# Performance work log

Hardware: AMD Instinct MI355X
Metric: run time of the kernel (lower is better)

## Reference

```python
import jax, jax.numpy as jnp
import numpy as np

NUM_USER, NUM_ITEM, NUM_TIME = 200000, 100000, 5000
P, Q, R = 32, 32, 32
N = 131072


def _xavier(key, shape):
    fan_in, fan_out = shape[0], int(np.prod(shape[1:]))
    limit = float(np.sqrt(6.0 / (fan_in + fan_out)))
    return jax.random.uniform(key, shape, dtype=jnp.float32, minval=-limit, maxval=limit)


def setup_inputs() -> dict:
    key = jax.random.key(0)
    k1, k2, k3, k4, k5, k6, k7 = jax.random.split(key, 7)
    return {
        "i_input": jax.random.randint(k1, (N,), 0, NUM_USER),
        "j_input": jax.random.randint(k2, (N,), 0, NUM_ITEM),
        "k_input": jax.random.randint(k3, (N,), 0, NUM_TIME),
        "user_embeddings": _xavier(k4, (NUM_USER, P)),
        "item_embeddings": _xavier(k5, (NUM_ITEM, Q)),
        "time_embeddings": _xavier(k6, (NUM_TIME, R)),
        "core_tensor": _xavier(k7, (P, Q, R)),
    }


def reference(i_input, j_input, k_input, user_embeddings, item_embeddings,
              time_embeddings, core_tensor):
    # Gather per-sample embeddings: [n,p], [n,q], [n,r]
    i_embeds = user_embeddings[i_input]
    j_embeds = item_embeddings[j_input]
    k_embeds = time_embeddings[k_input]
    # Fused Tucker contraction: never materialize the (n,p,q,r) outer product.
    # Mathematically identical to einsum('np,nq,nr,pqr->n', ...).
    t = jnp.einsum('np,pqr->nqr', i_embeds, core_tensor)  # [n,q,r]
    t = jnp.einsum('nqr,nq->nr', t, j_embeds)             # [n,r]
    return jnp.einsum('nr,nr->n', t, k_embeds)            # [n]
```

## Files before the change

kernel.cpp:

```cpp
#include <hip/hip_runtime.h>


#define BIN_CAP 128

__global__ __launch_bounds__(256) void build_H(const float* __restrict__ G,
                                               const float* __restrict__ W,
                                               float* __restrict__ H,
                                               int num_time) {
    const int pq4 = threadIdx.x;
    const int kbase = blockIdx.x * 8;

    float acc[8][4];
#pragma unroll
    for (int kk = 0; kk < 8; ++kk)
#pragma unroll
        for (int i = 0; i < 4; ++i) acc[kk][i] = 0.f;

#pragma unroll
    for (int r4 = 0; r4 < 8; ++r4) {
        float4 g[4];
#pragma unroll
        for (int i = 0; i < 4; ++i)
            g[i] = *(const float4*)(G + (size_t)(pq4 * 4 + i) * 32 + r4 * 4);
#pragma unroll
        for (int kk = 0; kk < 8; ++kk) {
            int k = kbase + kk;
            int kc = (k < num_time) ? k : (num_time - 1);
            float4 w = *(const float4*)(W + (size_t)kc * 32 + r4 * 4);
#pragma unroll
            for (int i = 0; i < 4; ++i)
                acc[kk][i] += g[i].x * w.x + g[i].y * w.y + g[i].z * w.z + g[i].w * w.w;
        }
    }

#pragma unroll
    for (int kk = 0; kk < 8; ++kk) {
        int k = kbase + kk;
        if (k < num_time) {
            float4 o = make_float4(acc[kk][0], acc[kk][1], acc[kk][2], acc[kk][3]);
            *(float4*)(H + (size_t)k * 1024 + pq4 * 4) = o;
        }
    }
}

__global__ __launch_bounds__(256) void scatter_k(const int* __restrict__ K,
                                                 const int* __restrict__ I,
                                                 const int* __restrict__ J,
                                                 int* __restrict__ counts,
                                                 int4* __restrict__ bins,
                                                 int* __restrict__ ovf_cnt,
                                                 int4* __restrict__ ovf,
                                                 int n) {
    for (int idx = blockIdx.x * blockDim.x + threadIdx.x; idx < n;
         idx += gridDim.x * blockDim.x) {
        int k = K[idx];
        int4 rec = make_int4(idx, I[idx], J[idx], k);
        int pos = atomicAdd(&counts[k], 1);
        if (pos < BIN_CAP) {
            bins[(size_t)k * BIN_CAP + pos] = rec;
        } else {
            int o = atomicAdd(ovf_cnt, 1);
            ovf[o] = rec;
        }
    }
}

__global__ __launch_bounds__(256) void tucker_eval_grouped(
        const float* __restrict__ U, const float* __restrict__ V,
        const float* __restrict__ H, const int* __restrict__ counts,
        const int4* __restrict__ bins, float* __restrict__ out,
        int num_time) {
    __shared__ float4 Hs4[4][256];
    const int wave = threadIdx.x >> 6;
    const int lane = threadIdx.x & 63;
    const int k = blockIdx.x * 4 + wave;
    const int qq = lane & 7;
    const int s8 = lane >> 3;

    int m = 0;
    if (k < num_time) {
        const float4* __restrict__ Hrow4 = (const float4*)(H + (size_t)k * 1024);
#pragma unroll
        for (int c = 0; c < 4; ++c)
            Hs4[wave][lane + 64 * c] = Hrow4[lane + 64 * c];
        m = counts[k];
        m = (m < BIN_CAP) ? m : BIN_CAP;
    }
    __syncthreads();
    if (k >= num_time || m == 0) return;

    const int iters = (m + 7) >> 3;
    const float4* __restrict__ Hw = Hs4[wave];

    for (int t = 0; t < iters; ++t) {
        const int s = t * 8 + s8;
        if (s < m) {
            int4 rec = bins[(size_t)k * BIN_CAP + s];
            const float4* __restrict__ Ur = (const float4*)(U + (size_t)rec.y * 32);
            float4 u[8];
#pragma unroll
            for (int p4 = 0; p4 < 8; ++p4) u[p4] = Ur[p4];
            float4 v4 = ((const float4*)(V + (size_t)rec.z * 32))[qq];

            float4 acc = make_float4(0.f, 0.f, 0.f, 0.f);
#pragma unroll
            for (int p4 = 0; p4 < 8; ++p4) {
                float4 h;
                h = Hw[(p4 * 4 + 0) * 8 + qq];
                acc.x += u[p4].x * h.x; acc.y += u[p4].x * h.y;
                acc.z += u[p4].x * h.z; acc.w += u[p4].x * h.w;
                h = Hw[(p4 * 4 + 1) * 8 + qq];
                acc.x += u[p4].y * h.x; acc.y += u[p4].y * h.y;
                acc.z += u[p4].y * h.z; acc.w += u[p4].y * h.w;
                h = Hw[(p4 * 4 + 2) * 8 + qq];
                acc.x += u[p4].z * h.x; acc.y += u[p4].z * h.y;
                acc.z += u[p4].z * h.z; acc.w += u[p4].z * h.w;
                h = Hw[(p4 * 4 + 3) * 8 + qq];
                acc.x += u[p4].w * h.x; acc.y += u[p4].w * h.y;
                acc.z += u[p4].w * h.z; acc.w += u[p4].w * h.w;
            }
            float sd = acc.x * v4.x + acc.y * v4.y + acc.z * v4.z + acc.w * v4.w;
            sd += __shfl_xor(sd, 1, 64);
            sd += __shfl_xor(sd, 2, 64);
            sd += __shfl_xor(sd, 4, 64);
            if (qq == 0) out[rec.x] = sd;
        }
    }
}

__global__ __launch_bounds__(256) void tucker_eval_overflow(
        const float* __restrict__ U, const float* __restrict__ V,
        const float* __restrict__ H, const int* __restrict__ ovf_cnt,
        const int4* __restrict__ ovf, float* __restrict__ out) {
    const int gwave = (int)((blockIdx.x * (unsigned)blockDim.x + threadIdx.x) >> 6);
    const int nwaves = (int)((gridDim.x * (unsigned)blockDim.x) >> 6);
    const int lane = threadIdx.x & 63;
    const int qq = lane & 7;
    const int pg = lane >> 3;
    const int cnt = *ovf_cnt;

    for (int s = gwave; s < cnt; s += nwaves) {
        int4 rec = ovf[s];
        const float4* __restrict__ Hrow = (const float4*)(H + (size_t)rec.w * 1024);
        const float* __restrict__ Ur = U + (size_t)rec.y * 32;

        float4 acc = make_float4(0.f, 0.f, 0.f, 0.f);
#pragma unroll
        for (int it = 0; it < 4; ++it) {
            float4 h = Hrow[lane + it * 64];
            float up = Ur[pg + it * 8];
            acc.x += up * h.x; acc.y += up * h.y;
            acc.z += up * h.z; acc.w += up * h.w;
        }
#pragma unroll
        for (int off = 8; off < 64; off <<= 1) {
            acc.x += __shfl_xor(acc.x, off, 64);
            acc.y += __shfl_xor(acc.y, off, 64);
            acc.z += __shfl_xor(acc.z, off, 64);
            acc.w += __shfl_xor(acc.w, off, 64);
        }
        float4 v4 = ((const float4*)(V + (size_t)rec.z * 32))[qq];
        float sd = acc.x * v4.x + acc.y * v4.y + acc.z * v4.z + acc.w * v4.w;
        sd += __shfl_xor(sd, 1, 64);
        sd += __shfl_xor(sd, 2, 64);
        sd += __shfl_xor(sd, 4, 64);
        if (lane == 0) out[rec.x] = sd;
    }
}

__global__ __launch_bounds__(256) void tucker_eval(const int* __restrict__ I,
                                                   const int* __restrict__ J,
                                                   const int* __restrict__ K,
                                                   const float* __restrict__ U,
                                                   const float* __restrict__ V,
                                                   const float* __restrict__ H,
                                                   float* __restrict__ out,
                                                   int n_samples) {
    const int wave = (int)((blockIdx.x * (unsigned)blockDim.x + threadIdx.x) >> 6);
    const int lane = threadIdx.x & 63;
    if (wave >= n_samples) return;
    const int i = I[wave];
    const int j = J[wave];
    const int k = K[wave];
    const int qq = lane & 7;
    const int pg = lane >> 3;
    const float4* __restrict__ Hrow = (const float4*)(H + (size_t)k * 1024);
    const float* __restrict__ Urow = U + (size_t)i * 32;
    float4 acc = make_float4(0.f, 0.f, 0.f, 0.f);
#pragma unroll
    for (int it = 0; it < 4; ++it) {
        float4 h = Hrow[lane + it * 64];
        float up = Urow[pg + it * 8];
        acc.x += up * h.x; acc.y += up * h.y;
        acc.z += up * h.z; acc.w += up * h.w;
    }
#pragma unroll
    for (int off = 8; off < 64; off <<= 1) {
        acc.x += __shfl_xor(acc.x, off, 64);
        acc.y += __shfl_xor(acc.y, off, 64);
        acc.z += __shfl_xor(acc.z, off, 64);
        acc.w += __shfl_xor(acc.w, off, 64);
    }
    float4 v4 = ((const float4*)(V + (size_t)j * 32))[qq];
    float s = acc.x * v4.x + acc.y * v4.y + acc.z * v4.z + acc.w * v4.w;
    s += __shfl_xor(s, 1, 64);
    s += __shfl_xor(s, 2, 64);
    s += __shfl_xor(s, 4, 64);
    if (lane == 0) out[wave] = s;
}

__global__ __launch_bounds__(256) void tucker_direct(const int* __restrict__ I,
                                                     const int* __restrict__ J,
                                                     const int* __restrict__ K,
                                                     const float* __restrict__ U,
                                                     const float* __restrict__ V,
                                                     const float* __restrict__ W,
                                                     const float* __restrict__ G,
                                                     float* __restrict__ out,
                                                     int n_samples) {
    __shared__ float Gc[4 * 32 * 32];
    const int n = blockIdx.x * blockDim.x + threadIdx.x;
    const bool active = (n < n_samples);
    int i = 0, j = 0, k = 0;
    if (active) { i = I[n]; j = J[n]; k = K[n]; }
    float4 w4[8];
#pragma unroll
    for (int r4 = 0; r4 < 8; ++r4)
        w4[r4] = ((const float4*)(W + (size_t)k * 32))[r4];
    float v[32];
#pragma unroll
    for (int q4 = 0; q4 < 8; ++q4) {
        float4 t = ((const float4*)(V + (size_t)j * 32))[q4];
        v[q4 * 4 + 0] = t.x; v[q4 * 4 + 1] = t.y;
        v[q4 * 4 + 2] = t.z; v[q4 * 4 + 3] = t.w;
    }
    const float* __restrict__ Urow = U + (size_t)i * 32;
    float acc = 0.f;
    for (int c = 0; c < 8; ++c) {
        __syncthreads();
#pragma unroll
        for (int t = 0; t < 4; ++t) {
            int idx = threadIdx.x + t * 256;
            ((float4*)Gc)[idx] = ((const float4*)(G + (size_t)c * 4096))[idx];
        }
        __syncthreads();
        for (int pp = 0; pp < 4; ++pp) {
            float up = Urow[c * 4 + pp];
#pragma unroll
            for (int q = 0; q < 32; ++q) {
                float t0 = 0.f;
#pragma unroll
                for (int r4 = 0; r4 < 8; ++r4) {
                    float4 g = ((const float4*)Gc)[pp * 256 + q * 8 + r4];
                    t0 += g.x * w4[r4].x + g.y * w4[r4].y + g.z * w4[r4].z + g.w * w4[r4].w;
                }
                acc += up * v[q] * t0;
            }
        }
    }
    if (active) out[n] = acc;
}

extern "C" void kernel_launch(void* const* d_in, const int* in_sizes, int n_in,
                              void* d_out, int out_size, void* d_ws, size_t ws_size,
                              hipStream_t stream) {
    const int*   I = (const int*)d_in[0];
    const int*   J = (const int*)d_in[1];
    const int*   K = (const int*)d_in[2];
    const float* U = (const float*)d_in[3];
    const float* V = (const float*)d_in[4];
    const float* W = (const float*)d_in[5];
    const float* G = (const float*)d_in[6];
    float* out = (float*)d_out;

    const int n_samples = in_sizes[0];
    const int num_time = in_sizes[5] / 32;

    const size_t h_bytes = (size_t)num_time * 1024 * sizeof(float);
    const size_t z_bytes = (size_t)(num_time + 1) * sizeof(int);
    const size_t z_pad = (z_bytes + 15) & ~(size_t)15;
    const size_t bins_bytes = (size_t)num_time * BIN_CAP * sizeof(int4);
    const size_t ovf_bytes = (size_t)n_samples * sizeof(int4);
    const size_t need_full = h_bytes + z_pad + bins_bytes + ovf_bytes;

    if (ws_size >= need_full) {
        float* H       = (float*)d_ws;
        int*   counts  = (int*)((char*)d_ws + h_bytes);
        int*   ovf_cnt = counts + num_time;
        int4*  bins    = (int4*)((char*)d_ws + h_bytes + z_pad);
        int4*  ovf     = (int4*)((char*)d_ws + h_bytes + z_pad + bins_bytes);

        hipMemsetAsync(counts, 0, z_bytes, stream);
        scatter_k<<<512, 256, 0, stream>>>(K, I, J, counts, bins, ovf_cnt, ovf,
                                           n_samples);
        build_H<<<(num_time + 7) / 8, 256, 0, stream>>>(G, W, H, num_time);
        tucker_eval_grouped<<<(num_time + 3) / 4, 256, 0, stream>>>(
            U, V, H, counts, bins, out, num_time);
        tucker_eval_overflow<<<64, 256, 0, stream>>>(U, V, H, ovf_cnt, ovf, out);
    } else if (ws_size >= h_bytes) {
        float* H = (float*)d_ws;
        build_H<<<(num_time + 7) / 8, 256, 0, stream>>>(G, W, H, num_time);
        const long long total_threads = (long long)n_samples * 64;
        tucker_eval<<<(int)((total_threads + 255) / 256), 256, 0, stream>>>(
            I, J, K, U, V, H, out, n_samples);
    } else {
        tucker_direct<<<(n_samples + 255) / 256, 256, 0, stream>>>(
            I, J, K, U, V, W, G, out, n_samples);
    }
}
```

Before: 136.6 us.

## Fuse scatter with H build and fold overflow pass into grouped eval

Merges the sample-binning scatter and the per-time H precompute into one launch, using a block-index split so the two independent jobs run concurrently. The overflow evaluation moves into the tail of the grouped eval kernel, dropping a separate launch. The grouped loop is also split into full 8-sample iterations plus one guarded remainder. Together these cut two kernel launches and the serialisation between them. The cost is a heterogeneous kernel whose register use is set by the heavier build path, and the overflow work now runs on every grouped block after its own bins are done.

Measured after the change: 137.1 us, median of 2. Within noise of the previous version (+0.4%).

```diff
diff --git a/kernel.cpp b/kernel.cpp
--- a/kernel.cpp
+++ b/kernel.cpp
@@ -3,64 +3,61 @@
 
 #define BIN_CAP 128
 
-__global__ __launch_bounds__(256) void build_H(const float* __restrict__ G,
-                                               const float* __restrict__ W,
-                                               float* __restrict__ H,
-                                               int num_time) {
-    const int pq4 = threadIdx.x;
-    const int kbase = blockIdx.x * 8;
-
-    float acc[8][4];
-#pragma unroll
-    for (int kk = 0; kk < 8; ++kk)
-#pragma unroll
-        for (int i = 0; i < 4; ++i) acc[kk][i] = 0.f;
-
-#pragma unroll
-    for (int r4 = 0; r4 < 8; ++r4) {
-        float4 g[4];
-#pragma unroll
-        for (int i = 0; i < 4; ++i)
-            g[i] = *(const float4*)(G + (size_t)(pq4 * 4 + i) * 32 + r4 * 4);
+__global__ __launch_bounds__(256) void scatter_build(
+        const int* __restrict__ K, const int* __restrict__ I,
+        const int* __restrict__ J, const float* __restrict__ G,
+        const float* __restrict__ W, int* __restrict__ counts,
+        int4* __restrict__ bins, int* __restrict__ ovf_cnt,
+        int4* __restrict__ ovf, float* __restrict__ H,
+        int n, int num_time, int n_scatter_blocks) {
+    if ((int)blockIdx.x < n_scatter_blocks) {
+        const int idx = blockIdx.x * 256 + threadIdx.x;
+        if (idx < n) {
+            int k = K[idx];
+            int4 rec = make_int4(idx, I[idx], J[idx], k);
+            int pos = atomicAdd(&counts[k], 1);
+            if (pos < BIN_CAP) {
+                bins[(size_t)k * BIN_CAP + pos] = rec;
+            } else {
+                int o = atomicAdd(ovf_cnt, 1);
+                ovf[o] = rec;
+            }
+        }
+    } else {
+        const int pq4 = threadIdx.x;
+        const int kbase = ((int)blockIdx.x - n_scatter_blocks) * 8;
+
+        float acc[8][4];
+#pragma unroll
+        for (int kk = 0; kk < 8; ++kk)
+#pragma unroll
+            for (int i = 0; i < 4; ++i) acc[kk][i] = 0.f;
+
+#pragma unroll
+        for (int r4 = 0; r4 < 8; ++r4) {
+            float4 g[4];
+#pragma unroll
+            for (int i = 0; i < 4; ++i)
+                g[i] = *(const float4*)(G + (size_t)(pq4 * 4 + i) * 32 + r4 * 4);
+#pragma unroll
+            for (int kk = 0; kk < 8; ++kk) {
+                int k = kbase + kk;
+                int kc = (k < num_time) ? k : (num_time - 1);
+                float4 w = *(const float4*)(W + (size_t)kc * 32 + r4 * 4);
+#pragma unroll
+                for (int i = 0; i < 4; ++i)
+                    acc[kk][i] += g[i].x * w.x + g[i].y * w.y +
+                                  g[i].z * w.z + g[i].w * w.w;
+            }
+        }
+
 #pragma unroll
         for (int kk = 0; kk < 8; ++kk) {
             int k = kbase + kk;
-            int kc = (k < num_time) ? k : (num_time - 1);
-            float4 w = *(const float4*)(W + (size_t)kc * 32 + r4 * 4);
-#pragma unroll
-            for (int i = 0; i < 4; ++i)
-                acc[kk][i] += g[i].x * w.x + g[i].y * w.y + g[i].z * w.z + g[i].w * w.w;
-        }
-    }
-
-#pragma unroll
-    for (int kk = 0; kk < 8; ++kk) {
-        int k = kbase + kk;
-        if (k < num_time) {
-            float4 o = make_float4(acc[kk][0], acc[kk][1], acc[kk][2], acc[kk][3]);
-            *(float4*)(H + (size_t)k * 1024 + pq4 * 4) = o;
-        }
-    }
-}
-
-__global__ __launch_bounds__(256) void scatter_k(const int* __restrict__ K,
-                                                 const int* __restrict__ I,
-                                                 const int* __restrict__ J,
-                                                 int* __restrict__ counts,
-                                                 int4* __restrict__ bins,
-                                                 int* __restrict__ ovf_cnt,
-                                                 int4* __restrict__ ovf,
-                                                 int n) {
-    for (int idx = blockIdx.x * blockDim.x + threadIdx.x; idx < n;
-         idx += gridDim.x * blockDim.x) {
-        int k = K[idx];
-        int4 rec = make_int4(idx, I[idx], J[idx], k);
-        int pos = atomicAdd(&counts[k], 1);
-        if (pos < BIN_CAP) {
-            bins[(size_t)k * BIN_CAP + pos] = rec;
-        } else {
-            int o = atomicAdd(ovf_cnt, 1);
-            ovf[o] = rec;
+            if (k < num_time) {
+                float4 o = make_float4(acc[kk][0], acc[kk][1], acc[kk][2], acc[kk][3]);
+                *(float4*)(H + (size_t)k * 1024 + pq4 * 4) = o;
+            }
         }
     }
 }
@@ -68,7 +65,8 @@
 __global__ __launch_bounds__(256) void tucker_eval_grouped(
         const float* __restrict__ U, const float* __restrict__ V,
         const float* __restrict__ H, const int* __restrict__ counts,
-        const int4* __restrict__ bins, float* __restrict__ out,
+        const int4* __restrict__ bins, const int* __restrict__ ovf_cnt,
+        const int4* __restrict__ ovf, float* __restrict__ out,
         int num_time) {
     __shared__ float4 Hs4[4][256];
     const int wave = threadIdx.x >> 6;
@@ -87,15 +85,15 @@
         m = (m < BIN_CAP) ? m : BIN_CAP;
     }
     __syncthreads();
-    if (k >= num_time || m == 0) return;
-
-    const int iters = (m + 7) >> 3;
-    const float4* __restrict__ Hw = Hs4[wave];
-
-    for (int t = 0; t < iters; ++t) {
-        const int s = t * 8 + s8;
-        if (s < m) {
-            int4 rec = bins[(size_t)k * BIN_CAP + s];
+
+    if (k < num_time && m > 0) {
+        const float4* __restrict__ Hw = Hs4[wave];
+        const int4* __restrict__ binsk = bins + (size_t)k * BIN_CAP;
+        const int full = m >> 3;
+
+        for (int t = 0; t < full; ++t) {
+            const int s = t * 8 + s8;
+            int4 rec = binsk[s];
             const float4* __restrict__ Ur = (const float4*)(U + (size_t)rec.y * 32);
             float4 u[8];
 #pragma unroll
@@ -125,46 +123,110 @@
             sd += __shfl_xor(sd, 4, 64);
             if (qq == 0) out[rec.x] = sd;
         }
-    }
-}
-
-__global__ __launch_bounds__(256) void tucker_eval_overflow(
-        const float* __restrict__ U, const float* __restrict__ V,
-        const float* __restrict__ H, const int* __restrict__ ovf_cnt,
-        const int4* __restrict__ ovf, float* __restrict__ out) {
-    const int gwave = (int)((blockIdx.x * (unsigned)blockDim.x + threadIdx.x) >> 6);
-    const int nwaves = (int)((gridDim.x * (unsigned)blockDim.x) >> 6);
-    const int lane = threadIdx.x & 63;
-    const int qq = lane & 7;
-    const int pg = lane >> 3;
+
+        const int s = full * 8 + s8;
+        if (s < m) {
+            int4 rec = binsk[s];
+            const float4* __restrict__ Ur = (const float4*)(U + (size_t)rec.y * 32);
+            float4 u[8];
+#pragma unroll
+            for (int p4 = 0; p4 < 8; ++p4) u[p4] = Ur[p4];
+            float4 v4 = ((const float4*)(V + (size_t)rec.z * 32))[qq];
+
+            float4 acc = make_float4(0.f, 0.f, 0.f, 0.f);
+#pragma unroll
+            for (int p4 = 0; p4 < 8; ++p4) {
+                float4 h;
+                h = Hw[(p4 * 4 + 0) * 8 + qq];
+                acc.x += u[p4].x * h.x; acc.y += u[p4].x * h.y;
+                acc.z += u[p4].x * h.z; acc.w += u[p4].x * h.w;
+                h = Hw[(p4 * 4 + 1) * 8 + qq];
+                acc.x += u[p4].y * h.x; acc.y += u[p4].y * h.y;
+                acc.z += u[p4].y * h.z; acc.w += u[p4].y * h.w;
+                h = Hw[(p4 * 4 + 2) * 8 + qq];
+                acc.x += u[p4].z * h.x; acc.y += u[p4].z * h.y;
+                acc.z += u[p4].z * h.z; acc.w += u[p4].z * h.w;
+                h = Hw[(p4 * 4 + 3) * 8 + qq];
+                acc.x += u[p4].w * h.x; acc.y += u[p4].w * h.y;
+                acc.z += u[p4].w * h.z; acc.w += u[p4].w * h.w;
+            }
+            float sd = acc.x * v4.x + acc.y * v4.y + acc.z * v4.z + acc.w * v4.w;
+            sd += __shfl_xor(sd, 1, 64);
+            sd += __shfl_xor(sd, 2, 64);
+            sd += __shfl_xor(sd, 4, 64);
+            if (qq == 0) out[rec.x] = sd;
+        }
+    }
+
     const int cnt = *ovf_cnt;
-
-    for (int s = gwave; s < cnt; s += nwaves) {
-        int4 rec = ovf[s];
-        const float4* __restrict__ Hrow = (const float4*)(H + (size_t)rec.w * 1024);
-        const float* __restrict__ Ur = U + (size_t)rec.y * 32;
-
-        float4 acc = make_float4(0.f, 0.f, 0.f, 0.f);
-#pragma unroll
-        for (int it = 0; it < 4; ++it) {
-            float4 h = Hrow[lane + it * 64];
-            float up = Ur[pg + it * 8];
-            acc.x += up * h.x; acc.y += up * h.y;
-            acc.z += up * h.z; acc.w += up * h.w;
-        }
-#pragma unroll
-        for (int off = 8; off < 64; off <<= 1) {
-            acc.x += __shfl_xor(acc.x, off, 64);
-            acc.y += __shfl_xor(acc.y, off, 64);
-            acc.z += __shfl_xor(acc.z, off, 64);
-            acc.w += __shfl_xor(acc.w, off, 64);
-        }
-        float4 v4 = ((const float4*)(V + (size_t)rec.z * 32))[qq];
-        float sd = acc.x * v4.x + acc.y * v4.y + acc.z * v4.z + acc.w * v4.w;
-        sd += __shfl_xor(sd, 1, 64);
-        sd += __shfl_xor(sd, 2, 64);
-        sd += __shfl_xor(sd, 4, 64);
-        if (lane == 0) out[rec.x] = sd;
+    if (cnt > 0) {
+        const int pg = lane >> 3;
+        const int gwave = blockIdx.x * 4 + wave;
+        const int nwaves = gridDim.x * 4;
+        for (int s = gwave; s < cnt; s += nwaves) {
+            int4 rec = ovf[s];
+            const float4* __restrict__ Hrow = (const float4*)(H + (size_t)rec.w * 1024);
+            const float* __restrict__ Ur = U + (size_t)rec.y * 32;
+
+            float4 acc = make_float4(0.f, 0.f, 0.f, 0.f);
+#pragma unroll
+            for (int it = 0; it < 4; ++it) {
+                float4 h = Hrow[lane + it * 64];
+                float up = Ur[pg + it * 8];
+                acc.x += up * h.x; acc.y += up * h.y;
+                acc.z += up * h.z; acc.w += up * h.w;
+            }
+#pragma unroll
+            for (int off = 8; off < 64; off <<= 1) {
+                acc.x += __shfl_xor(acc.x, off, 64);
+                acc.y += __shfl_xor(acc.y, off, 64);
+                acc.z += __shfl_xor(acc.z, off, 64);
+                acc.w += __shfl_xor(acc.w, off, 64);
+            }
+            float4 v4 = ((const float4*)(V + (size_t)rec.z * 32))[qq];
+            float sd = acc.x * v4.x + acc.y * v4.y + acc.z * v4.z + acc.w * v4.w;
+            sd += __shfl_xor(sd, 1, 64);
+            sd += __shfl_xor(sd, 2, 64);
+            sd += __shfl_xor(sd, 4, 64);
+            if (lane == 0) out[rec.x] = sd;
+        }
+    }
+}
+
+__global__ __launch_bounds__(256) void build_H(const float* __restrict__ G,
+                                               const float* __restrict__ W,
+                                               float* __restrict__ H,
+                                               int num_time) {
+    const int pq4 = threadIdx.x;
+    const int kbase = blockIdx.x * 8;
+    float acc[8][4];
+#pragma unroll
+    for (int kk = 0; kk < 8; ++kk)
+#pragma unroll
+        for (int i = 0; i < 4; ++i) acc[kk][i] = 0.f;
+#pragma unroll
+    for (int r4 = 0; r4 < 8; ++r4) {
+        float4 g[4];
+#pragma unroll
+        for (int i = 0; i < 4; ++i)
+            g[i] = *(const float4*)(G + (size_t)(pq4 * 4 + i) * 32 + r4 * 4);
+#pragma unroll
+        for (int kk = 0; kk < 8; ++kk) {
+            int k = kbase + kk;
+            int kc = (k < num_time) ? k : (num_time - 1);
+            float4 w = *(const float4*)(W + (size_t)kc * 32 + r4 * 4);
+#pragma unroll
+            for (int i = 0; i < 4; ++i)
+                acc[kk][i] += g[i].x * w.x + g[i].y * w.y + g[i].z * w.z + g[i].w * w.w;
+        }
+    }
+#pragma unroll
+    for (int kk = 0; kk < 8; ++kk) {
+        int k = kbase + kk;
+        if (k < num_time) {
+            float4 o = make_float4(acc[kk][0], acc[kk][1], acc[kk][2], acc[kk][3]);
+            *(float4*)(H + (size_t)k * 1024 + pq4 * 4) = o;
+        }
     }
 }
 
@@ -290,13 +352,15 @@
         int4*  bins    = (int4*)((char*)d_ws + h_bytes + z_pad);
         int4*  ovf     = (int4*)((char*)d_ws + h_bytes + z_pad + bins_bytes);
 
+        const int sb = (n_samples + 255) / 256;
+        const int bb = (num_time + 7) / 8;
+
         hipMemsetAsync(counts, 0, z_bytes, stream);
-        scatter_k<<<512, 256, 0, stream>>>(K, I, J, counts, bins, ovf_cnt, ovf,
-                                           n_samples);
-        build_H<<<(num_time + 7) / 8, 256, 0, stream>>>(G, W, H, num_time);
+        scatter_build<<<sb + bb, 256, 0, stream>>>(K, I, J, G, W, counts, bins,
+                                                   ovf_cnt, ovf, H, n_samples,
+                                                   num_time, sb);
         tucker_eval_grouped<<<(num_time + 3) / 4, 256, 0, stream>>>(
-            U, V, H, counts, bins, out, num_time);
-        tucker_eval_overflow<<<64, 256, 0, stream>>>(U, V, H, ovf_cnt, ovf, out);
+            U, V, H, counts, bins, ovf_cnt, ovf, out, num_time);
     } else if (ws_size >= h_bytes) {
         float* H = (float*)d_ws;
         build_H<<<(num_time + 7) / 8, 256, 0, stream>>>(G, W, H, num_time);
```
